# Performance work log

Hardware: AMD Instinct MI355X
Metric: run time of the kernel (lower is better)

The kernel has to match this reference:

```python
import jax, jax.numpy as jnp
import numpy as np

N_NODES = 50000
N_EDGES = 800000
IN_CH = 128
OUT_CH = 32
HID = 2 * OUT_CH  # 64


def setup_inputs() -> dict:
    key = jax.random.key(0)
    ks = jax.random.split(key, 8)
    x = jax.random.normal(ks[0], (N_NODES, IN_CH), dtype=jnp.float32)
    edge_index = jax.random.randint(ks[1], (2, N_EDGES), 0, N_NODES, dtype=jnp.int32)
    s1 = 1.0 / np.sqrt(IN_CH)
    s2 = 1.0 / np.sqrt(HID)
    W1 = jax.random.normal(ks[2], (IN_CH, HID), dtype=jnp.float32) * s1
    b1 = jnp.zeros((HID,), dtype=jnp.float32)
    W_mu = jax.random.normal(ks[3], (HID, OUT_CH), dtype=jnp.float32) * s2
    b_mu = jnp.zeros((OUT_CH,), dtype=jnp.float32)
    W_logstd = jax.random.normal(ks[4], (HID, OUT_CH), dtype=jnp.float32) * s2
    b_logstd = jnp.zeros((OUT_CH,), dtype=jnp.float32)
    return {"x": x, "edge_index": edge_index, "W1": W1, "b1": b1,
            "W_mu": W_mu, "b_mu": b_mu, "W_logstd": W_logstd, "b_logstd": b_logstd}


def _gcn_norm(edge_index, n, dtype):
    # PyG GCNConv: add self-loops, symmetric normalization D^-1/2 A D^-1/2
    loops = jnp.arange(n, dtype=edge_index.dtype)
    src = jnp.concatenate([edge_index[0], loops])
    dst = jnp.concatenate([edge_index[1], loops])
    deg = jax.ops.segment_sum(jnp.ones_like(dst, dtype=dtype), dst, num_segments=n)
    deg_inv_sqrt = jnp.where(deg > 0, jax.lax.rsqrt(deg), 0.0)
    norm = deg_inv_sqrt[src] * deg_inv_sqrt[dst]  # [E+N]
    return src, dst, norm


def _gcn_conv(x, W, b, src, dst, norm, n):
    h = x @ W                        # transform first (in >= out)
    msg = h[src] * norm[:, None]     # gather + scale, [E+N, out]
    out = jax.ops.segment_sum(msg, dst, num_segments=n)
    return out + b


def reference(x, edge_index, W1, b1, W_mu, b_mu, W_logstd, b_logstd):
    n = x.shape[0]
    src, dst, norm = _gcn_norm(edge_index, n, x.dtype)
    h = jax.nn.relu(_gcn_conv(x, W1, b1, src, dst, norm, n))
    mu = _gcn_conv(h, W_mu, b_mu, src, dst, norm, n)
    logstd = _gcn_conv(h, W_logstd, b_logstd, src, dst, norm, n)
    return mu, logstd
```

## Files before the change

### kernel.cpp

```cpp
#include <hip/hip_runtime.h>
#include <hip/hip_fp16.h>

#define N_NODES 50000
#define N_EDGES 800000
#define IN_CH 128
#define HID 64
#define OUT_CH 32
#define CAP 64
#define ZROW N_NODES
#define PART_SZ 6250

union H4 { uint2 u; __half2 h[2]; };

__global__ __launch_bounds__(256) void k_scatter(const int* __restrict__ ei,
                                                 int* cur, unsigned short* __restrict__ pk,
                                                 unsigned* zA, unsigned* zB) {
    if (blockIdx.x == 0) {
        int t = threadIdx.x;
        if (t < 32) zA[t] = 0u;
        else if (t < 64) zB[t - 32] = 0u;
    }
    int part = blockIdx.x & 7;
    int g = (blockIdx.x >> 3) * 256 + threadIdx.x;
    if (g >= N_EDGES / 2) return;
    int2 dd = ((const int2*)(ei + N_EDGES))[g];
    bool a0 = (unsigned)(dd.x - part * PART_SZ) < (unsigned)PART_SZ;
    bool a1 = (unsigned)(dd.y - part * PART_SZ) < (unsigned)PART_SZ;
    if (!a0 && !a1) return;
    int2 ss = ((const int2*)ei)[g];
    if (a0) {
        int pos = (dd.x << 6) + atomicAdd(&cur[dd.x], 1);
        pk[pos] = (unsigned short)ss.x;
    }
    if (a1) {
        int pos = (dd.y << 6) + atomicAdd(&cur[dd.y], 1);
        pk[pos] = (unsigned short)ss.y;
    }
}

__global__ __launch_bounds__(256) void k_mm1(const float* __restrict__ x,
                                             const float* __restrict__ W1,
                                             const int* __restrict__ cur,
                                             __half* __restrict__ t1) {
    __shared__ float4 ws[64 * 16];
    __shared__ float  xsT[64 * 64];
    int t = threadIdx.x;
    int n0 = blockIdx.x * 64;
    int lane = t & 63, wv_ = t >> 6;
    int ni = lane >> 2;
    int cq = ((lane & 3) << 2) + wv_;
    const float4* W4 = (const float4*)W1;
    const float4* x4 = (const float4*)x;
    float4 acc0 = {0,0,0,0}, acc1 = acc0, acc2 = acc0, acc3 = acc0;
#pragma unroll
    for (int kt = 0; kt < 2; ++kt) {
        __syncthreads();
#pragma unroll
        for (int i = 0; i < 4; ++i) {
            int L = i * 256 + t;
            ws[L] = W4[kt * 1024 + L];
            int n = L >> 4, q = L & 15;
            int ng = n0 + n; if (ng >= N_NODES) ng = N_NODES - 1;
            float4 v = x4[ng * 32 + kt * 16 + q];
            int fb = q * 256 + (((n >> 2) ^ q) << 2) + (n & 3);
            xsT[fb]       = v.x;
            xsT[fb + 64]  = v.y;
            xsT[fb + 128] = v.z;
            xsT[fb + 192] = v.w;
        }
        __syncthreads();
        const float4* xsT4 = (const float4*)xsT;
#pragma unroll 8
        for (int k = 0; k < 64; ++k) {
            float4 xv = xsT4[k * 16 + (ni ^ (k >> 2))];
            float4 wvv = ws[k * 16 + cq];
            acc0.x += xv.x * wvv.x; acc0.y += xv.x * wvv.y; acc0.z += xv.x * wvv.z; acc0.w += xv.x * wvv.w;
            acc1.x += xv.y * wvv.x; acc1.y += xv.y * wvv.y; acc1.z += xv.y * wvv.z; acc1.w += xv.y * wvv.w;
            acc2.x += xv.z * wvv.x; acc2.y += xv.z * wvv.y; acc2.z += xv.z * wvv.z; acc2.w += xv.z * wvv.w;
            acc3.x += xv.w * wvv.x; acc3.y += xv.w * wvv.y; acc3.z += xv.w * wvv.z; acc3.w += xv.w * wvv.w;
        }
    }
    int nb = n0 + 4 * ni;
    if (nb < N_NODES) {
        int4 c4 = *(const int4*)(cur + nb);
        float d0 = rsqrtf((float)c4.x + 1.0f);
        float d1 = rsqrtf((float)c4.y + 1.0f);
        float d2 = rsqrtf((float)c4.z + 1.0f);
        float d3 = rsqrtf((float)c4.w + 1.0f);
        uint2* o2 = (uint2*)t1;
        H4 v;
        v.h[0] = __floats2half2_rn(d0 * acc0.x, d0 * acc0.y);
        v.h[1] = __floats2half2_rn(d0 * acc0.z, d0 * acc0.w);
        o2[(nb + 0) * 16 + cq] = v.u;
        v.h[0] = __floats2half2_rn(d1 * acc1.x, d1 * acc1.y);
        v.h[1] = __floats2half2_rn(d1 * acc1.z, d1 * acc1.w);
        o2[(nb + 1) * 16 + cq] = v.u;
        v.h[0] = __floats2half2_rn(d2 * acc2.x, d2 * acc2.y);
        v.h[1] = __floats2half2_rn(d2 * acc2.z, d2 * acc2.w);
        o2[(nb + 2) * 16 + cq] = v.u;
        v.h[0] = __floats2half2_rn(d3 * acc3.x, d3 * acc3.y);
        v.h[1] = __floats2half2_rn(d3 * acc3.z, d3 * acc3.w);
        o2[(nb + 3) * 16 + cq] = v.u;
    }
}

__global__ __launch_bounds__(256) void k_agg(const unsigned short* __restrict__ pk,
                                             const int* __restrict__ cur,
                                             const __half* __restrict__ in,
                                             const float* __restrict__ bias,
                                             __half* __restrict__ out,
                                             int apply_relu) {
    int w = (blockIdx.x * 256 + threadIdx.x) >> 6;
    if (w >= N_NODES) return;
    int lane = threadIdx.x & 63;
    int eg = lane >> 3, cs = lane & 7;
    int cnt = __builtin_amdgcn_readfirstlane(cur[w]);
    int beg = w << 6, end = beg + cnt;
    const uint4* __restrict__ inv = (const uint4*)in;
    float acc[8] = {0,0,0,0,0,0,0,0};
#pragma unroll 2
    for (int base = beg; base < end; base += 8) {
        int je = base + eg;
        int s = (je < end) ? (int)pk[je] : ZROW;
        uint4 r = inv[s * 8 + cs];
        const __half2* h2 = (const __half2*)&r;
        float2 f;
        f = __half22float2(h2[0]); acc[0] += f.x; acc[1] += f.y;
        f = __half22float2(h2[1]); acc[2] += f.x; acc[3] += f.y;
        f = __half22float2(h2[2]); acc[4] += f.x; acc[5] += f.y;
        f = __half22float2(h2[3]); acc[6] += f.x; acc[7] += f.y;
    }
#pragma unroll
    for (int m = 8; m <= 32; m <<= 1)
#pragma unroll
        for (int i = 0; i < 8; ++i) acc[i] += __shfl_xor(acc[i], m, 64);
    if (eg == 0) {
        uint4 sr = inv[w * 8 + cs];
        const __half2* sh = (const __half2*)&sr;
        float2 f;
        f = __half22float2(sh[0]); acc[0] += f.x; acc[1] += f.y;
        f = __half22float2(sh[1]); acc[2] += f.x; acc[3] += f.y;
        f = __half22float2(sh[2]); acc[4] += f.x; acc[5] += f.y;
        f = __half22float2(sh[3]); acc[6] += f.x; acc[7] += f.y;
        float dw = rsqrtf((float)cnt + 1.0f);
        if (apply_relu) {
            float4 b0 = ((const float4*)bias)[2 * cs];
            float4 b1v = ((const float4*)bias)[2 * cs + 1];
            acc[0] = dw * fmaxf(dw * acc[0] + b0.x, 0.f);
            acc[1] = dw * fmaxf(dw * acc[1] + b0.y, 0.f);
            acc[2] = dw * fmaxf(dw * acc[2] + b0.z, 0.f);
            acc[3] = dw * fmaxf(dw * acc[3] + b0.w, 0.f);
            acc[4] = dw * fmaxf(dw * acc[4] + b1v.x, 0.f);
            acc[5] = dw * fmaxf(dw * acc[5] + b1v.y, 0.f);
            acc[6] = dw * fmaxf(dw * acc[6] + b1v.z, 0.f);
            acc[7] = dw * fmaxf(dw * acc[7] + b1v.w, 0.f);
        } else {
#pragma unroll
            for (int i = 0; i < 8; ++i) acc[i] *= dw;
        }
        __half2 o[4];
        o[0] = __floats2half2_rn(acc[0], acc[1]);
        o[1] = __floats2half2_rn(acc[2], acc[3]);
        o[2] = __floats2half2_rn(acc[4], acc[5]);
        o[3] = __floats2half2_rn(acc[6], acc[7]);
        ((uint4*)out)[w * 8 + cs] = *(const uint4*)o;
    }
}

__global__ __launch_bounds__(256) void k_mm2(const __half* __restrict__ agg2,
                                             const float* __restrict__ Wmu,
                                             const float* __restrict__ bmu,
                                             const float* __restrict__ Wls,
                                             const float* __restrict__ bls,
                                             float* __restrict__ out) {
    __shared__ float4 ws[64 * 16];
    __shared__ float  xsT[64 * 64];
    int t = threadIdx.x;
    int n0 = blockIdx.x * 64;
    int lane = t & 63, wv_ = t >> 6;
    int ni = lane >> 2;
    int cq = ((lane & 3) << 2) + wv_;
    const float4* Wm4 = (const float4*)Wmu;
    const float4* Wl4 = (const float4*)Wls;
    const uint2*  x2  = (const uint2*)agg2;
#pragma unroll
    for (int i = 0; i < 4; ++i) {
        int L = i * 256 + t;
        int k = L >> 4, c = L & 15;
        ws[L] = (c < 8) ? Wm4[k * 8 + c] : Wl4[k * 8 + (c - 8)];
        int n = L >> 4, q = L & 15;
        int ng = n0 + n; if (ng >= N_NODES) ng = N_NODES - 1;
        H4 hv; hv.u = x2[ng * 16 + q];
        float2 f0 = __half22float2(hv.h[0]), f1 = __half22float2(hv.h[1]);
        int fb = q * 256 + (((n >> 2) ^ q) << 2) + (n & 3);
        xsT[fb]       = f0.x;
        xsT[fb + 64]  = f0.y;
        xsT[fb + 128] = f1.x;
        xsT[fb + 192] = f1.y;
    }
    float4 b = (cq < 8) ? ((const float4*)bmu)[cq] : ((const float4*)bls)[cq - 8];
    float4 acc0 = b, acc1 = b, acc2 = b, acc3 = b;
    __syncthreads();
    const float4* xsT4 = (const float4*)xsT;
#pragma unroll 8
    for (int k = 0; k < 64; ++k) {
        float4 xv = xsT4[k * 16 + (ni ^ (k >> 2))];
        float4 wvv = ws[k * 16 + cq];
        acc0.x += xv.x * wvv.x; acc0.y += xv.x * wvv.y; acc0.z += xv.x * wvv.z; acc0.w += xv.x * wvv.w;
        acc1.x += xv.y * wvv.x; acc1.y += xv.y * wvv.y; acc1.z += xv.y * wvv.z; acc1.w += xv.y * wvv.w;
        acc2.x += xv.z * wvv.x; acc2.y += xv.z * wvv.y; acc2.z += xv.z * wvv.z; acc2.w += xv.z * wvv.w;
        acc3.x += xv.w * wvv.x; acc3.y += xv.w * wvv.y; acc3.z += xv.w * wvv.z; acc3.w += xv.w * wvv.w;
    }
    int nb = n0 + 4 * ni;
    if (nb < N_NODES) {
        float4* o4 = (float4*)out;
        long base_off = (cq < 8) ? 0 : (long)N_NODES * 8;
        int cq8 = cq & 7;
        o4[base_off + (long)(nb + 0) * 8 + cq8] = acc0;
        o4[base_off + (long)(nb + 1) * 8 + cq8] = acc1;
        o4[base_off + (long)(nb + 2) * 8 + cq8] = acc2;
        o4[base_off + (long)(nb + 3) * 8 + cq8] = acc3;
    }
}

extern "C" void kernel_launch(void* const* d_in, const int* in_sizes, int n_in,
                              void* d_out, int out_size, void* d_ws, size_t ws_size,
                              hipStream_t stream) {
    const float* x   = (const float*)d_in[0];
    const int*   ei  = (const int*)  d_in[1];
    const float* W1  = (const float*)d_in[2];
    const float* b1  = (const float*)d_in[3];
    const float* Wmu = (const float*)d_in[4];
    const float* bmu = (const float*)d_in[5];
    const float* Wls = (const float*)d_in[6];
    const float* bls = (const float*)d_in[7];
    float* out = (float*)d_out;

    int*   cur  = (int*)d_ws;
    unsigned short* pk = (unsigned short*)((int*)d_ws + 50176);
    __half* bufA = (__half*)((int*)d_ws + 1650176);
    __half* bufB = (__half*)((int*)d_ws + 3250304);
    __half* bufC = (__half*)((int*)d_ws + 4850432);

    hipMemsetAsync(d_ws, 0, 200000, stream);
    k_scatter <<<1563 * 8, 256, 0, stream>>>(ei, cur, pk,
                   (unsigned*)(bufA + (size_t)ZROW * HID),
                   (unsigned*)(bufB + (size_t)ZROW * HID));
    k_mm1 <<<782, 256, 0, stream>>>(x, W1, cur, bufA);
    k_agg <<<12500, 256, 0, stream>>>(pk, cur, bufA, b1, bufB, 1);
    k_agg <<<12500, 256, 0, stream>>>(pk, cur, bufB, nullptr, bufC, 0);
    k_mm2 <<<782, 256, 0, stream>>>(bufC, Wmu, bmu, Wls, bls, out);
}
```

Baseline: 196.3 us.

## Split adjacency by source half and add cache-warming passes before aggregation

Each destination's neighbor list is split into two 32-slot buckets by whether the source index falls in the lower or upper half of the nodes, with separate counters. The aggregation then walks the low-half sources first and the high-half sources second, aiming for better cache locality in the gathers. Separate warm-up kernels stream the feature buffer before each aggregation, meant to pull it into the last-level cache. The cost is two extra launches and a full read of each buffer, and each bucket is now capped at 32 neighbors per half.

New measurement: 203.4 us. +3.6%, slower.

```diff
diff --git a/kernel.cpp b/kernel.cpp
--- a/kernel.cpp
+++ b/kernel.cpp
@@ -6,7 +6,7 @@
 #define IN_CH 128
 #define HID 64
 #define OUT_CH 32
-#define CAP 64
+#define HALF_N 25000
 #define ZROW N_NODES
 #define PART_SZ 6250
 
@@ -29,13 +29,25 @@
     if (!a0 && !a1) return;
     int2 ss = ((const int2*)ei)[g];
     if (a0) {
-        int pos = (dd.x << 6) + atomicAdd(&cur[dd.x], 1);
+        int b = (ss.x >= HALF_N);
+        int pos = (dd.x << 6) + (b << 5) + atomicAdd(&cur[b * N_NODES + dd.x], 1);
         pk[pos] = (unsigned short)ss.x;
     }
     if (a1) {
-        int pos = (dd.y << 6) + atomicAdd(&cur[dd.y], 1);
+        int b = (ss.y >= HALF_N);
+        int pos = (dd.y << 6) + (b << 5) + atomicAdd(&cur[b * N_NODES + dd.y], 1);
         pk[pos] = (unsigned short)ss.y;
     }
+}
+
+__global__ __launch_bounds__(256) void k_warm(const float4* __restrict__ p, int n4) {
+    float4 a = {0, 0, 0, 0};
+    for (int i = blockIdx.x * 256 + threadIdx.x; i < n4; i += gridDim.x * 256) {
+        float4 v = p[i];
+        a.x += v.x; a.y += v.y; a.z += v.z; a.w += v.w;
+    }
+    float s = a.x + a.y + a.z + a.w;
+    asm volatile("" :: "v"(s));
 }
 
 __global__ __launch_bounds__(256) void k_mm1(const float* __restrict__ x,
@@ -82,11 +94,12 @@
     }
     int nb = n0 + 4 * ni;
     if (nb < N_NODES) {
-        int4 c4 = *(const int4*)(cur + nb);
-        float d0 = rsqrtf((float)c4.x + 1.0f);
-        float d1 = rsqrtf((float)c4.y + 1.0f);
-        float d2 = rsqrtf((float)c4.z + 1.0f);
-        float d3 = rsqrtf((float)c4.w + 1.0f);
+        int4 a4 = *(const int4*)(cur + nb);
+        int4 b4 = *(const int4*)(cur + N_NODES + nb);
+        float d0 = rsqrtf((float)(a4.x + b4.x) + 1.0f);
+        float d1 = rsqrtf((float)(a4.y + b4.y) + 1.0f);
+        float d2 = rsqrtf((float)(a4.z + b4.z) + 1.0f);
+        float d3 = rsqrtf((float)(a4.w + b4.w) + 1.0f);
         uint2* o2 = (uint2*)t1;
         H4 v;
         v.h[0] = __floats2half2_rn(d0 * acc0.x, d0 * acc0.y);
@@ -114,14 +127,27 @@
     if (w >= N_NODES) return;
     int lane = threadIdx.x & 63;
     int eg = lane >> 3, cs = lane & 7;
-    int cnt = __builtin_amdgcn_readfirstlane(cur[w]);
-    int beg = w << 6, end = beg + cnt;
+    int c0 = __builtin_amdgcn_readfirstlane(cur[w]);
+    int c1 = __builtin_amdgcn_readfirstlane(cur[N_NODES + w]);
+    int rowb = w << 6;
     const uint4* __restrict__ inv = (const uint4*)in;
     float acc[8] = {0,0,0,0,0,0,0,0};
 #pragma unroll 2
-    for (int base = beg; base < end; base += 8) {
+    for (int base = 0; base < c0; base += 8) {
         int je = base + eg;
-        int s = (je < end) ? (int)pk[je] : ZROW;
+        int s = (je < c0) ? (int)pk[rowb + je] : ZROW;
+        uint4 r = inv[s * 8 + cs];
+        const __half2* h2 = (const __half2*)&r;
+        float2 f;
+        f = __half22float2(h2[0]); acc[0] += f.x; acc[1] += f.y;
+        f = __half22float2(h2[1]); acc[2] += f.x; acc[3] += f.y;
+        f = __half22float2(h2[2]); acc[4] += f.x; acc[5] += f.y;
+        f = __half22float2(h2[3]); acc[6] += f.x; acc[7] += f.y;
+    }
+#pragma unroll 2
+    for (int base = 0; base < c1; base += 8) {
+        int je = base + eg;
+        int s = (je < c1) ? (int)pk[rowb + 32 + je] : ZROW;
         uint4 r = inv[s * 8 + cs];
         const __half2* h2 = (const __half2*)&r;
         float2 f;
@@ -142,7 +168,7 @@
         f = __half22float2(sh[1]); acc[2] += f.x; acc[3] += f.y;
         f = __half22float2(sh[2]); acc[4] += f.x; acc[5] += f.y;
         f = __half22float2(sh[3]); acc[6] += f.x; acc[7] += f.y;
-        float dw = rsqrtf((float)cnt + 1.0f);
+        float dw = rsqrtf((float)(c0 + c1) + 1.0f);
         if (apply_relu) {
             float4 b0 = ((const float4*)bias)[2 * cs];
             float4 b1v = ((const float4*)bias)[2 * cs + 1];
@@ -237,17 +263,19 @@
     float* out = (float*)d_out;
 
     int*   cur  = (int*)d_ws;
-    unsigned short* pk = (unsigned short*)((int*)d_ws + 50176);
-    __half* bufA = (__half*)((int*)d_ws + 1650176);
-    __half* bufB = (__half*)((int*)d_ws + 3250304);
-    __half* bufC = (__half*)((int*)d_ws + 4850432);
-
-    hipMemsetAsync(d_ws, 0, 200000, stream);
+    unsigned short* pk = (unsigned short*)((int*)d_ws + 100096);
+    __half* bufA = (__half*)((int*)d_ws + 1700096);
+    __half* bufB = (__half*)((int*)d_ws + 3300128);
+    __half* bufC = (__half*)((int*)d_ws + 4900160);
+
+    hipMemsetAsync(d_ws, 0, 400000, stream);
     k_scatter <<<1563 * 8, 256, 0, stream>>>(ei, cur, pk,
                    (unsigned*)(bufA + (size_t)ZROW * HID),
                    (unsigned*)(bufB + (size_t)ZROW * HID));
-    k_mm1 <<<782, 256, 0, stream>>>(x, W1, cur, bufA);
-    k_agg <<<12500, 256, 0, stream>>>(pk, cur, bufA, b1, bufB, 1);
-    k_agg <<<12500, 256, 0, stream>>>(pk, cur, bufB, nullptr, bufC, 0);
-    k_mm2 <<<782, 256, 0, stream>>>(bufC, Wmu, bmu, Wls, bls, out);
-}
+    k_mm1  <<<782, 256, 0, stream>>>(x, W1, cur, bufA);
+    k_warm <<<1024, 256, 0, stream>>>((const float4*)bufA, 400008);
+    k_agg  <<<12500, 256, 0, stream>>>(pk, cur, bufA, b1, bufB, 1);
+    k_warm <<<1024, 256, 0, stream>>>((const float4*)bufB, 400008);
+    k_agg  <<<12500, 256, 0, stream>>>(pk, cur, bufB, nullptr, bufC, 0);
+    k_mm2  <<<782, 256, 0, stream>>>(bufC, Wmu, bmu, Wls, bls, out);
+}
```
